# Optimization experiments

Hardware: AMD Instinct MI355X
Metric: run time of the kernel (lower is better)

Reference implementation:

```python
import jax, jax.numpy as jnp
import numpy as np

NEG_SLOPE = 0.2  # PyG GATConv default LeakyReLU slope
EPS = 1e-16


def gat_conv(x, edge_index, W, a_src, a_dst, bias, heads, out_ch, concat):
    """PyG-style GATConv (eval mode, add_self_loops=True).
    x: [N, F_in], edge_index: [2, E] (row0=source, row1=target).
    """
    N = x.shape[0]
    loops = jnp.arange(N, dtype=edge_index.dtype)
    src = jnp.concatenate([edge_index[0], loops])  # [E+N]
    dst = jnp.concatenate([edge_index[1], loops])

    h = (x @ W).reshape(N, heads, out_ch)            # [N, H, C]
    alpha_s = jnp.sum(h * a_src, axis=-1)            # [N, H]
    alpha_d = jnp.sum(h * a_dst, axis=-1)            # [N, H]

    e = alpha_s[src] + alpha_d[dst]                  # [E+N, H]
    e = jnp.where(e > 0, e, NEG_SLOPE * e)           # LeakyReLU

    # segment softmax over incoming edges of each target node
    m = jax.ops.segment_max(e, dst, num_segments=N)  # [N, H]
    m = jnp.where(jnp.isfinite(m), m, 0.0)
    ex = jnp.exp(e - m[dst])
    s = jax.ops.segment_sum(ex, dst, num_segments=N)  # [N, H]
    alpha = ex / (s[dst] + EPS)                       # [E+N, H]

    msg = h[src] * alpha[:, :, None]                  # [E+N, H, C]
    out = jax.ops.segment_sum(msg, dst, num_segments=N)  # [N, H, C]

    if concat:
        out = out.reshape(N, heads * out_ch)
    else:
        out = out.mean(axis=1)
    return out + bias


def setup_inputs() -> dict:
    key = jax.random.key(0)
    ks = jax.random.split(key, 10)
    N, E, F_in = 50000, 1000000, 128
    H, C, OUT = 4, 16, 40
    x = jax.random.normal(ks[0], (N, F_in), dtype=jnp.float32)
    edge_index = jax.random.randint(ks[1], (2, E), 0, N, dtype=jnp.int64)
    sc1 = 1.0 / np.sqrt(F_in)
    sc2 = 1.0 / np.sqrt(H * C)
    return {
        "x": x,
        "edge_index": edge_index,
        "W1": jax.random.normal(ks[2], (F_in, H * C), dtype=jnp.float32) * sc1,
        "a_src1": jax.random.normal(ks[3], (H, C), dtype=jnp.float32) * sc2,
        "a_dst1": jax.random.normal(ks[4], (H, C), dtype=jnp.float32) * sc2,
        "b1": jnp.zeros((H * C,), dtype=jnp.float32),
        "W2": jax.random.normal(ks[5], (H * C, OUT), dtype=jnp.float32) * sc2,
        "a_src2": jax.random.normal(ks[6], (1, OUT), dtype=jnp.float32) * 0.15,
        "a_dst2": jax.random.normal(ks[7], (1, OUT), dtype=jnp.float32) * 0.15,
        "b2": jnp.zeros((OUT,), dtype=jnp.float32),
    }


def reference(x, edge_index, W1, a_src1, a_dst1, b1, W2, a_src2, a_dst2, b2):
    h = gat_conv(x, edge_index, W1, a_src1, a_dst1, b1, heads=4, out_ch=16, concat=True)
    h = jax.nn.elu(h)  # dropout is identity in eval mode
    out = gat_conv(h, edge_index, W2, a_src2, a_dst2, b2, heads=1, out_ch=40, concat=False)
    return out
```

## Files before the change

### kernel.cpp

```cpp
#include <hip/hip_runtime.h>

#define NEG_SLOPE 0.2f
#define GAT_EPS 1e-16f
#define NB 256
#define SB 512
#define DPB 128

__device__ __forceinline__ float leaky(float e){ return e > 0.f ? e : NEG_SLOPE * e; }

__device__ __forceinline__ unsigned bf2(float a, float b){
  unsigned ua = __float_as_uint(a); ua += 0x7FFFu + ((ua >> 16) & 1u);
  unsigned ub = __float_as_uint(b); ub += 0x7FFFu + ((ub >> 16) & 1u);
  return (ua >> 16) | (ub & 0xFFFF0000u);
}
__device__ __forceinline__ float bflo(unsigned v){ return __uint_as_float(v << 16); }
__device__ __forceinline__ float bfhi(unsigned v){ return __uint_as_float(v & 0xFFFF0000u); }

__global__ __launch_bounds__(256) void k_g1c(const float* __restrict__ x,
                                             const float* __restrict__ W,
                                             const float* __restrict__ a_src,
                                             const float* __restrict__ a_dst,
                                             unsigned* __restrict__ h1b,
                                             float* __restrict__ as1,
                                             float* __restrict__ ad1, int N,
                                             const int* __restrict__ ei,
                                             int* __restrict__ bcnt,
                                             int E, int T, int nbin, int chunk, int G1){
  if ((int)blockIdx.x >= G1){
    __shared__ int lh[SB];
    const int b = (int)blockIdx.x - G1;
    const int lo = b*chunk;
    const int hi = min(lo + chunk, T);
    for (int i = threadIdx.x; i < nbin; i += 256) lh[i] = 0;
    __syncthreads();
    for (int i = lo + (int)threadIdx.x; i < hi; i += 256){
      int dst = (i < E) ? ei[E+i] : (i - E);
      atomicAdd(&lh[dst >> 7], 1);
    }
    __syncthreads();
    for (int i = threadIdx.x; i < nbin; i += 256) bcnt[b*SB + i] = lh[i];
    return;
  }
  __shared__ float Ws[128*64];
  __shared__ float xs[64*20];
  const int t = threadIdx.x;
  const int n0 = blockIdx.x * 64;
  for (int i = t; i < 128*64/4; i += 256) ((float4*)Ws)[i] = ((const float4*)W)[i];
  const int ct = t & 15;
  const int rt = t >> 4;
  const int lr = t >> 2;
  const int lq = t & 3;
  const bool rok = (n0 + lr) < N;
  const float* xrow = x + (size_t)(n0 + lr)*128 + lq*4;
  float acc[4][4];
#pragma unroll
  for (int i = 0; i < 4; i++)
#pragma unroll
    for (int j = 0; j < 4; j++) acc[i][j] = 0.f;

  for (int kc = 0; kc < 8; kc++){
    float4 xv = {0.f,0.f,0.f,0.f};
    if (rok) xv = *(const float4*)(xrow + kc*16);
    __syncthreads();
    *(float4*)(xs + lr*20 + lq*4) = xv;
    __syncthreads();
#pragma unroll
    for (int kk = 0; kk < 16; kk++){
      const int k = kc*16 + kk;
      float4 wv = *(const float4*)(Ws + k*64 + ct*4);
      float x0 = xs[(rt*4+0)*20 + kk];
      float x1 = xs[(rt*4+1)*20 + kk];
      float x2 = xs[(rt*4+2)*20 + kk];
      float x3 = xs[(rt*4+3)*20 + kk];
      acc[0][0] += x0*wv.x; acc[0][1] += x0*wv.y; acc[0][2] += x0*wv.z; acc[0][3] += x0*wv.w;
      acc[1][0] += x1*wv.x; acc[1][1] += x1*wv.y; acc[1][2] += x1*wv.z; acc[1][3] += x1*wv.w;
      acc[2][0] += x2*wv.x; acc[2][1] += x2*wv.y; acc[2][2] += x2*wv.z; acc[2][3] += x2*wv.w;
      acc[3][0] += x3*wv.x; acc[3][1] += x3*wv.y; acc[3][2] += x3*wv.z; acc[3][3] += x3*wv.w;
    }
  }
  const int h = ct >> 2;
  const float4 asv = *(const float4*)(a_src + ct*4);
  const float4 adv = *(const float4*)(a_dst + ct*4);
#pragma unroll
  for (int i = 0; i < 4; i++){
    int n = n0 + rt*4 + i;
    float ss = acc[i][0]*asv.x + acc[i][1]*asv.y + acc[i][2]*asv.z + acc[i][3]*asv.w;
    float dd = acc[i][0]*adv.x + acc[i][1]*adv.y + acc[i][2]*adv.z + acc[i][3]*adv.w;
    ss += __shfl_xor(ss, 1); ss += __shfl_xor(ss, 2);
    dd += __shfl_xor(dd, 1); dd += __shfl_xor(dd, 2);
    if (n < N){
      h1b[(size_t)n*32 + ct*2 + 0] = bf2(acc[i][0], acc[i][1]);
      h1b[(size_t)n*32 + ct*2 + 1] = bf2(acc[i][2], acc[i][3]);
      if ((ct & 3) == 0){
        as1[(size_t)n*4 + h] = ss;
        ad1[(size_t)n*4 + h] = dd;
      }
    }
  }
}

__global__ __launch_bounds__(512) void k_scan(const int* __restrict__ bcnt,
                                              int* __restrict__ qbase,
                                              int* __restrict__ qtot, int nbin){
  const int w = blockIdx.x*8 + ((int)threadIdx.x >> 6);
  const int l = (int)threadIdx.x & 63;
  if (w >= nbin) return;
  int vals[NB/64];
  int s = 0;
#pragma unroll
  for (int j = 0; j < NB/64; j++){
    vals[j] = bcnt[((l*(NB/64)) + j)*SB + w];
    s += vals[j];
  }
  int incl = s;
#pragma unroll
  for (int off = 1; off < 64; off <<= 1){
    int t = __shfl_up(incl, off);
    if (l >= off) incl += t;
  }
  int run = incl - s;
#pragma unroll
  for (int j = 0; j < NB/64; j++){
    qbase[((l*(NB/64)) + j)*SB + w] = run;
    run += vals[j];
  }
  if (l == 63) qtot[w] = run;
}

__global__ __launch_bounds__(256) void k_scat(const int* __restrict__ ei,
                                              const int* __restrict__ qbase,
                                              unsigned* __restrict__ queue,
                                              int E, int T, int nbin, int cap, int chunk){
  __shared__ int qb[SB];
  const int b = blockIdx.x;
  const int lo = b*chunk;
  const int hi = min(lo + chunk, T);
  for (int i = threadIdx.x; i < nbin; i += 256) qb[i] = qbase[b*SB + i];
  __syncthreads();
  for (int i = lo + (int)threadIdx.x; i < hi; i += 256){
    int src, dst;
    if (i < E){ src = ei[i]; dst = ei[E+i]; }
    else      { src = dst = i - E; }
    const int bin = dst >> 7;
    const int pos = atomicAdd(&qb[bin], 1);
    if (pos < cap)
      queue[(size_t)bin*cap + pos] = ((unsigned)dst << 16) | (unsigned)src;
  }
}

__global__ __launch_bounds__(256) void k_fillq(const int* __restrict__ qtot,
                                               const unsigned* __restrict__ queue,
                                               int* __restrict__ cnt,
                                               unsigned short* __restrict__ slots,
                                               int cap, int N){
  __shared__ int lcnt[DPB];
  const int sb = blockIdx.x;
  const int lo = sb * DPB;
  const int hi = min(lo + DPB, N);
  for (int i = threadIdx.x; i < DPB; i += 256) lcnt[i] = 0;
  __syncthreads();
  const int qn = min(qtot[sb], cap);
  const unsigned* q = queue + (size_t)sb*cap;
  for (int i = (int)threadIdx.x; i < qn; i += 256){
    const unsigned p = q[i];
    const int d = (int)(p >> 16) - lo;
    if ((unsigned)d < (unsigned)DPB){
      const int pos = atomicAdd(&lcnt[d], 1);
      if (pos < 64) slots[(size_t)(lo + d)*64 + pos] = (unsigned short)(p & 0xFFFFu);
    }
  }
  __syncthreads();
  for (int i = threadIdx.x; i < hi - lo; i += 256) cnt[lo + i] = lcnt[i];
}

__global__ __launch_bounds__(256) void k_edge1(const int* __restrict__ cnt,
     const unsigned short* __restrict__ slots, const float* __restrict__ as1,
     const float* __restrict__ ad1, const unsigned* __restrict__ h1b,
     const float* __restrict__ b1, float* __restrict__ g1, int N){
  int wave = (blockIdx.x << 2) + (threadIdx.x >> 6);
  if (wave >= N) return;
  const int lane = threadIdx.x & 63;
  const int e8 = lane >> 3;
  const int c8 = lane & 7;
  const int h  = c8 >> 1;
  const int deg = min(cnt[wave], 64);
  const int base = wave << 6;
  const float4 ad = *(const float4*)(ad1 + (size_t)wave*4);
  const float adh = (h==0)?ad.x:(h==1)?ad.y:(h==2)?ad.z:ad.w;

  float4 accA = {0.f,0.f,0.f,0.f};
  float4 accB = {0.f,0.f,0.f,0.f};
  float lsum = 0.f;
  for (int jb = 0; jb < deg; jb += 8){
    int slot = jb + e8;
    int s = 0; float p = 0.f;
    if (slot < deg){
      s = slots[base + slot];
      p = __expf(leaky(as1[(size_t)s*4 + h] + adh));
    }
    uint4 w = *(const uint4*)(h1b + (size_t)s*32 + c8*4);
    accA.x += p * bflo(w.x); accA.y += p * bfhi(w.x);
    accA.z += p * bflo(w.y); accA.w += p * bfhi(w.y);
    accB.x += p * bflo(w.z); accB.y += p * bfhi(w.z);
    accB.z += p * bflo(w.w); accB.w += p * bfhi(w.w);
    lsum += p;
  }
#pragma unroll
  for (int off = 8; off < 64; off <<= 1){
    accA.x += __shfl_xor(accA.x, off); accA.y += __shfl_xor(accA.y, off);
    accA.z += __shfl_xor(accA.z, off); accA.w += __shfl_xor(accA.w, off);
    accB.x += __shfl_xor(accB.x, off); accB.y += __shfl_xor(accB.y, off);
    accB.z += __shfl_xor(accB.z, off); accB.w += __shfl_xor(accB.w, off);
  }
  lsum += __shfl_xor(lsum, 1);
  lsum += __shfl_xor(lsum, 8);
  lsum += __shfl_xor(lsum, 16);
  lsum += __shfl_xor(lsum, 32);
  lsum *= 0.5f;

  if (e8 == 0){
    float inv = 1.f / (lsum + GAT_EPS);
    const float4 bA = *(const float4*)(b1 + c8*8);
    const float4 bB = *(const float4*)(b1 + c8*8 + 4);
    float4 vA, vB;
    vA.x = accA.x*inv + bA.x; vA.y = accA.y*inv + bA.y;
    vA.z = accA.z*inv + bA.z; vA.w = accA.w*inv + bA.w;
    vB.x = accB.x*inv + bB.x; vB.y = accB.y*inv + bB.y;
    vB.z = accB.z*inv + bB.z; vB.w = accB.w*inv + bB.w;
    vA.x = vA.x > 0.f ? vA.x : (__expf(vA.x) - 1.f);
    vA.y = vA.y > 0.f ? vA.y : (__expf(vA.y) - 1.f);
    vA.z = vA.z > 0.f ? vA.z : (__expf(vA.z) - 1.f);
    vA.w = vA.w > 0.f ? vA.w : (__expf(vA.w) - 1.f);
    vB.x = vB.x > 0.f ? vB.x : (__expf(vB.x) - 1.f);
    vB.y = vB.y > 0.f ? vB.y : (__expf(vB.y) - 1.f);
    vB.z = vB.z > 0.f ? vB.z : (__expf(vB.z) - 1.f);
    vB.w = vB.w > 0.f ? vB.w : (__expf(vB.w) - 1.f);
    *(float4*)(g1 + (size_t)wave*64 + c8*8)     = vA;
    *(float4*)(g1 + (size_t)wave*64 + c8*8 + 4) = vB;
  }
}

__global__ __launch_bounds__(256) void k_gemm2(const float* __restrict__ g1,
                                               const float* __restrict__ W2,
                                               const float* __restrict__ a_src,
                                               const float* __restrict__ a_dst,
                                               unsigned* __restrict__ h2lo,
                                               unsigned* __restrict__ h2hi,
                                               float* __restrict__ as2,
                                               float* __restrict__ ad2, int N){
  __shared__ float Ws[64*40];
  __shared__ float xs[32*64];
  const int t = threadIdx.x;
  const int n0 = blockIdx.x * 32;
  for (int i = t; i < 64*40; i += 256) Ws[i] = W2[i];
  for (int i = t; i < 32*64; i += 256){
    int n = n0 + (i >> 6);
    xs[i] = (n < N) ? g1[(size_t)n*64 + (i & 63)] : 0.f;
  }
  __syncthreads();
  const int c  = t & 63;
  const int ng = t >> 6;
  const bool act = (c < 40);
  float acc[8] = {0,0,0,0,0,0,0,0};
  if (act){
    for (int k = 0; k < 64; k++){
      float w = Ws[k*40 + c];
#pragma unroll
      for (int r = 0; r < 8; r++) acc[r] += xs[(ng*8+r)*64 + k] * w;
    }
  }
  const float av = act ? a_src[c] : 0.f;
  const float bv = act ? a_dst[c] : 0.f;
#pragma unroll
  for (int r = 0; r < 8; r++){
    int n = n0 + ng*8 + r;
    float po = __shfl_xor(acc[r], 1);
    if ((c & 1) == 0 && act && n < N){
      unsigned pk = bf2(acc[r], po);
      if (c < 32) h2lo[(size_t)n*16 + (c >> 1)] = pk;
      else        h2hi[(size_t)n*4  + ((c-32) >> 1)] = pk;
    }
    float ss = acc[r]*av, dd = acc[r]*bv;
#pragma unroll
    for (int off = 1; off < 64; off <<= 1){
      ss += __shfl_xor(ss, off);
      dd += __shfl_xor(dd, off);
    }
    if (c == 0 && n < N){ as2[n] = ss; ad2[n] = dd; }
  }
}

__global__ __launch_bounds__(256) void k_edge2(const int* __restrict__ cnt,
     const unsigned short* __restrict__ slots, const float* __restrict__ as2,
     const float* __restrict__ ad2, const unsigned* __restrict__ h2lo,
     const unsigned* __restrict__ h2hi, const float* __restrict__ b2,
     float* __restrict__ out, int N){
  int wave = (blockIdx.x << 2) + (threadIdx.x >> 6);
  if (wave >= N) return;
  const int lane = threadIdx.x & 63;
  const int e8 = lane >> 3;
  const int c8 = lane & 7;
  const int deg = min(cnt[wave], 64);
  const int base = wave << 6;
  const float adw = ad2[wave];

  float4 accA = {0.f,0.f,0.f,0.f};
  float4 accB = {0.f,0.f,0.f,0.f};
  float lsum = 0.f;
  for (int jb = 0; jb < deg; jb += 8){
    int slot = jb + e8;
    int s = 0; float p = 0.f;
    if (slot < deg){
      s = slots[base + slot];
      p = __expf(leaky(as2[s] + adw));
    }
    lsum += p;
    if (c8 < 5){
      uint4 w = (c8 < 4) ? *(const uint4*)(h2lo + (size_t)s*16 + c8*4)
                         : *(const uint4*)(h2hi + (size_t)s*4);
      accA.x += p * bflo(w.x); accA.y += p * bfhi(w.x);
      accA.z += p * bflo(w.y); accA.w += p * bfhi(w.y);
      accB.x += p * bflo(w.z); accB.y += p * bfhi(w.z);
      accB.z += p * bflo(w.w); accB.w += p * bfhi(w.w);
    }
  }
#pragma unroll
  for (int off = 8; off < 64; off <<= 1){
    accA.x += __shfl_xor(accA.x, off); accA.y += __shfl_xor(accA.y, off);
    accA.z += __shfl_xor(accA.z, off); accA.w += __shfl_xor(accA.w, off);
    accB.x += __shfl_xor(accB.x, off); accB.y += __shfl_xor(accB.y, off);
    accB.z += __shfl_xor(accB.z, off); accB.w += __shfl_xor(accB.w, off);
  }
#pragma unroll
  for (int off = 1; off < 64; off <<= 1) lsum += __shfl_xor(lsum, off);
  lsum *= 0.125f;

  if (e8 == 0 && c8 < 5){
    float inv = 1.f / (lsum + GAT_EPS);
    const float4 bA = *(const float4*)(b2 + c8*8);
    const float4 bB = *(const float4*)(b2 + c8*8 + 4);
    float4 vA, vB;
    vA.x = accA.x*inv + bA.x; vA.y = accA.y*inv + bA.y;
    vA.z = accA.z*inv + bA.z; vA.w = accA.w*inv + bA.w;
    vB.x = accB.x*inv + bB.x; vB.y = accB.y*inv + bB.y;
    vB.z = accB.z*inv + bB.z; vB.w = accB.w*inv + bB.w;
    *(float4*)(out + (size_t)wave*40 + c8*8)     = vA;
    *(float4*)(out + (size_t)wave*40 + c8*8 + 4) = vB;
  }
}

extern "C" void kernel_launch(void* const* d_in, const int* in_sizes, int n_in,
                              void* d_out, int out_size, void* d_ws, size_t ws_size,
                              hipStream_t stream){
  const float* x    = (const float*)d_in[0];
  const int*   ei   = (const int*)d_in[1];
  const float* W1   = (const float*)d_in[2];
  const float* a_s1 = (const float*)d_in[3];
  const float* a_d1 = (const float*)d_in[4];
  const float* b1   = (const float*)d_in[5];
  const float* W2   = (const float*)d_in[6];
  const float* a_s2 = (const float*)d_in[7];
  const float* a_d2 = (const float*)d_in[8];
  const float* b2   = (const float*)d_in[9];
  float* out = (float*)d_out;

  const int N = in_sizes[0] / 128;
  const int E = in_sizes[1] / 2;
  const int T = E + N;
  const int nbin = (N + DPB - 1) / DPB;
  const int chunk = (T + NB - 1) / NB;
  const int cap = ((T/nbin + 1024) + 255) & ~255;
  const int G1 = (N + 63) / 64;

  float* ws = (float*)d_ws;
  unsigned* h1b  = (unsigned*)ws; ws += (size_t)N*32;
  unsigned* h2lo = (unsigned*)ws; ws += (size_t)N*16;
  unsigned* h2hi = (unsigned*)ws; ws += (size_t)N*4;
  float* as1 = ws;  ws += (size_t)N*4;
  float* ad1 = ws;  ws += (size_t)N*4;
  float* g1  = ws;  ws += (size_t)N*64;
  float* as2 = ws;  ws += (size_t)N;
  float* ad2 = ws;  ws += (size_t)N;
  int* cnt   = (int*)ws;          ws += (size_t)N;
  int* bcnt  = (int*)ws;          ws += (size_t)NB*SB;
  int* qbase = (int*)ws;          ws += (size_t)NB*SB;
  int* qtot  = (int*)ws;          ws += SB;
  unsigned short* slots = (unsigned short*)ws; ws += (size_t)N*32;
  unsigned* queue = (unsigned*)ws; ws += (size_t)nbin*cap;

  hipLaunchKernelGGL(k_g1c, dim3(G1 + NB), dim3(256), 0, stream,
                     x, W1, a_s1, a_d1, h1b, as1, ad1, N,
                     ei, bcnt, E, T, nbin, chunk, G1);
  hipLaunchKernelGGL(k_scan, dim3((nbin+7)/8), dim3(512), 0, stream, bcnt, qbase, qtot, nbin);
  hipLaunchKernelGGL(k_scat, dim3(NB), dim3(256), 0, stream, ei, qbase, queue, E, T, nbin, cap, chunk);
  hipLaunchKernelGGL(k_fillq, dim3(nbin), dim3(256), 0, stream, qtot, queue, cnt, slots, cap, N);

  hipLaunchKernelGGL(k_edge1, dim3((N+3)/4), dim3(256), 0, stream,
                     cnt, slots, as1, ad1, h1b, b1, g1, N);

  hipLaunchKernelGGL(k_gemm2, dim3((N+31)/32), dim3(256), 0, stream,
                     g1, W2, a_s2, a_d2, h2lo, h2hi, as2, ad2, N);
  hipLaunchKernelGGL(k_edge2, dim3((N+3)/4), dim3(256), 0, stream,
                     cnt, slots, as2, ad2, h2lo, h2hi, b2, out, N);
}
```

Measured before the change: 226.3 us.

## Compute layer-1 projection with split-bf16 MFMA instead of FP32 FMA

Replaces the scalar FP32 register-tiled GEMM for x@W1 in the fused first kernel with MFMA 16x16x32 bf16 instructions. Both operands are split into hi/lo bf16 parts and three MFMAs are accumulated to keep near-FP32 accuracy. W is pre-split into a packed shared-memory layout, and the attention-score reductions are redone with cross-lane shuffles. The histogram branch reuses the same shared buffer. The intent is to cut the ALU cost of the projection, at the price of extra conversion work and a small accuracy change.

```diff
diff --git a/kernel.cpp b/kernel.cpp
--- a/kernel.cpp
+++ b/kernel.cpp
@@ -6,6 +6,9 @@
 #define SB 512
 #define DPB 128
 
+typedef __attribute__((ext_vector_type(8))) short bf16x8;
+typedef __attribute__((ext_vector_type(4))) float f32x4;
+
 __device__ __forceinline__ float leaky(float e){ return e > 0.f ? e : NEG_SLOPE * e; }
 
 __device__ __forceinline__ unsigned bf2(float a, float b){
@@ -15,6 +18,10 @@
 }
 __device__ __forceinline__ float bflo(unsigned v){ return __uint_as_float(v << 16); }
 __device__ __forceinline__ float bfhi(unsigned v){ return __uint_as_float(v & 0xFFFF0000u); }
+__device__ __forceinline__ unsigned short bfh(float f){
+  unsigned u = __float_as_uint(f); u += 0x7FFFu + ((u >> 16) & 1u);
+  return (unsigned short)(u >> 16);
+}
 
 __global__ __launch_bounds__(256) void k_g1c(const float* __restrict__ x,
                                              const float* __restrict__ W,
@@ -26,8 +33,9 @@
                                              const int* __restrict__ ei,
                                              int* __restrict__ bcnt,
                                              int E, int T, int nbin, int chunk, int G1){
+  __shared__ unsigned Wf[8192];
   if ((int)blockIdx.x >= G1){
-    __shared__ int lh[SB];
+    int* lh = (int*)Wf;
     const int b = (int)blockIdx.x - G1;
     const int lo = b*chunk;
     const int hi = min(lo + chunk, T);
@@ -41,62 +49,101 @@
     for (int i = threadIdx.x; i < nbin; i += 256) bcnt[b*SB + i] = lh[i];
     return;
   }
-  __shared__ float Ws[128*64];
-  __shared__ float xs[64*20];
   const int t = threadIdx.x;
   const int n0 = blockIdx.x * 64;
-  for (int i = t; i < 128*64/4; i += 256) ((float4*)Ws)[i] = ((const float4*)W)[i];
-  const int ct = t & 15;
-  const int rt = t >> 4;
-  const int lr = t >> 2;
-  const int lq = t & 3;
-  const bool rok = (n0 + lr) < N;
-  const float* xrow = x + (size_t)(n0 + lr)*128 + lq*4;
-  float acc[4][4];
-#pragma unroll
-  for (int i = 0; i < 4; i++)
-#pragma unroll
-    for (int j = 0; j < 4; j++) acc[i][j] = 0.f;
-
-  for (int kc = 0; kc < 8; kc++){
-    float4 xv = {0.f,0.f,0.f,0.f};
-    if (rok) xv = *(const float4*)(xrow + kc*16);
-    __syncthreads();
-    *(float4*)(xs + lr*20 + lq*4) = xv;
-    __syncthreads();
-#pragma unroll
-    for (int kk = 0; kk < 16; kk++){
-      const int k = kc*16 + kk;
-      float4 wv = *(const float4*)(Ws + k*64 + ct*4);
-      float x0 = xs[(rt*4+0)*20 + kk];
-      float x1 = xs[(rt*4+1)*20 + kk];
-      float x2 = xs[(rt*4+2)*20 + kk];
-      float x3 = xs[(rt*4+3)*20 + kk];
-      acc[0][0] += x0*wv.x; acc[0][1] += x0*wv.y; acc[0][2] += x0*wv.z; acc[0][3] += x0*wv.w;
-      acc[1][0] += x1*wv.x; acc[1][1] += x1*wv.y; acc[1][2] += x1*wv.z; acc[1][3] += x1*wv.w;
-      acc[2][0] += x2*wv.x; acc[2][1] += x2*wv.y; acc[2][2] += x2*wv.z; acc[2][3] += x2*wv.w;
-      acc[3][0] += x3*wv.x; acc[3][1] += x3*wv.y; acc[3][2] += x3*wv.z; acc[3][3] += x3*wv.w;
-    }
-  }
-  const int h = ct >> 2;
-  const float4 asv = *(const float4*)(a_src + ct*4);
-  const float4 adv = *(const float4*)(a_dst + ct*4);
-#pragma unroll
-  for (int i = 0; i < 4; i++){
-    int n = n0 + rt*4 + i;
-    float ss = acc[i][0]*asv.x + acc[i][1]*asv.y + acc[i][2]*asv.z + acc[i][3]*asv.w;
-    float dd = acc[i][0]*adv.x + acc[i][1]*adv.y + acc[i][2]*adv.z + acc[i][3]*adv.w;
-    ss += __shfl_xor(ss, 1); ss += __shfl_xor(ss, 2);
-    dd += __shfl_xor(dd, 1); dd += __shfl_xor(dd, 2);
-    if (n < N){
-      h1b[(size_t)n*32 + ct*2 + 0] = bf2(acc[i][0], acc[i][1]);
-      h1b[(size_t)n*32 + ct*2 + 1] = bf2(acc[i][2], acc[i][3]);
-      if ((ct & 3) == 0){
-        as1[(size_t)n*4 + h] = ss;
-        ad1[(size_t)n*4 + h] = dd;
-      }
-    }
-  }
+  for (int i = t; i < 8192; i += 256){
+    const int e = i >> 10, kcct = (i >> 6) & 15, ln = i & 63;
+    const int k = (kcct >> 2)*32 + (ln >> 4)*8 + e;
+    const int c = (kcct & 3)*16 + (ln & 15);
+    const float wv = W[k*64 + c];
+    const unsigned short hi = bfh(wv);
+    const unsigned short lo = bfh(wv - __uint_as_float((unsigned)hi << 16));
+    Wf[i] = ((unsigned)hi << 16) | (unsigned)lo;
+  }
+  __syncthreads();
+  const int w  = t >> 6;
+  const int l  = t & 63;
+  const int kg = l >> 4;
+  const int col = l & 15;
+  const int row = n0 + w*16 + col;
+  const bool rok = row < N;
+  const float* xrow = x + (size_t)row*128;
+
+  f32x4 acc0 = {0.f,0.f,0.f,0.f}, acc1 = acc0, acc2 = acc0, acc3 = acc0;
+
+#pragma unroll
+  for (int kc = 0; kc < 4; kc++){
+    float xa[8];
+    if (rok){
+      float4 va = *(const float4*)(xrow + kc*32 + kg*8);
+      float4 vb = *(const float4*)(xrow + kc*32 + kg*8 + 4);
+      xa[0]=va.x; xa[1]=va.y; xa[2]=va.z; xa[3]=va.w;
+      xa[4]=vb.x; xa[5]=vb.y; xa[6]=vb.z; xa[7]=vb.w;
+    } else {
+#pragma unroll
+      for (int e = 0; e < 8; e++) xa[e] = 0.f;
+    }
+    bf16x8 Ahi, Alo;
+#pragma unroll
+    for (int e = 0; e < 8; e++){
+      const unsigned short hi = bfh(xa[e]);
+      Ahi[e] = (short)hi;
+      Alo[e] = (short)bfh(xa[e] - __uint_as_float((unsigned)hi << 16));
+    }
+#define DO_CT(ACC, CT)                                                          \
+    {                                                                           \
+      bf16x8 Bhi, Blo;                                                          \
+      _Pragma("unroll")                                                         \
+      for (int e = 0; e < 8; e++){                                              \
+        const unsigned u = Wf[((e*16) + kc*4 + (CT))*64 + l];                   \
+        Bhi[e] = (short)(u >> 16);                                              \
+        Blo[e] = (short)(u & 0xFFFFu);                                          \
+      }                                                                         \
+      ACC = __builtin_amdgcn_mfma_f32_16x16x32_bf16(Ahi, Bhi, ACC, 0, 0, 0);    \
+      ACC = __builtin_amdgcn_mfma_f32_16x16x32_bf16(Ahi, Blo, ACC, 0, 0, 0);    \
+      ACC = __builtin_amdgcn_mfma_f32_16x16x32_bf16(Alo, Bhi, ACC, 0, 0, 0);    \
+    }
+    DO_CT(acc0, 0)
+    DO_CT(acc1, 1)
+    DO_CT(acc2, 2)
+    DO_CT(acc3, 3)
+#undef DO_CT
+  }
+
+#define EPI(ACC, CT)                                                            \
+  {                                                                             \
+    const float a0 = ACC[0], a1 = ACC[1], a2 = ACC[2], a3 = ACC[3];             \
+    const float p0 = __shfl_xor(a0, 1), p1 = __shfl_xor(a1, 1),                 \
+                p2 = __shfl_xor(a2, 1), p3 = __shfl_xor(a3, 1);                 \
+    if ((col & 1) == 0){                                                        \
+      const int wi = (CT)*8 + (col >> 1);                                       \
+      int n = n0 + w*16 + kg*4;                                                 \
+      if (n+0 < N) h1b[(size_t)(n+0)*32 + wi] = bf2(a0, p0);                    \
+      if (n+1 < N) h1b[(size_t)(n+1)*32 + wi] = bf2(a1, p1);                    \
+      if (n+2 < N) h1b[(size_t)(n+2)*32 + wi] = bf2(a2, p2);                    \
+      if (n+3 < N) h1b[(size_t)(n+3)*32 + wi] = bf2(a3, p3);                    \
+    }                                                                           \
+    const float asc = a_src[(CT)*16 + col];                                     \
+    const float adc = a_dst[(CT)*16 + col];                                     \
+    _Pragma("unroll")                                                           \
+    for (int j = 0; j < 4; j++){                                                \
+      const float aj = (j==0)?a0:(j==1)?a1:(j==2)?a2:a3;                        \
+      float ss = aj*asc, dd = aj*adc;                                           \
+      ss += __shfl_xor(ss, 1); ss += __shfl_xor(ss, 2);                         \
+      ss += __shfl_xor(ss, 4); ss += __shfl_xor(ss, 8);                         \
+      dd += __shfl_xor(dd, 1); dd += __shfl_xor(dd, 2);                         \
+      dd += __shfl_xor(dd, 4); dd += __shfl_xor(dd, 8);                         \
+      if (col == 0){                                                            \
+        const int n = n0 + w*16 + kg*4 + j;                                     \
+        if (n < N){ as1[(size_t)n*4 + (CT)] = ss; ad1[(size_t)n*4 + (CT)] = dd; } \
+      }                                                                         \
+    }                                                                           \
+  }
+  EPI(acc0, 0)
+  EPI(acc1, 1)
+  EPI(acc2, 2)
+  EPI(acc3, 3)
+#undef EPI
 }
 
 __global__ __launch_bounds__(512) void k_scan(const int* __restrict__ bcnt,
```

Measured after the change: 226.0 us. Within noise of the previous version (-0.2%).
